# Performance work log

Hardware: AMD Instinct MI355X
Metric: run time of the kernel (lower is better)

Reference implementation:

```python
import jax, jax.numpy as jnp
import numpy as np

NUM_AGES = 100
FEAT_DIM = 512
BATCH = 4096
TEMPERATURE = 0.1
EPS = 1e-6


def setup_inputs() -> dict:
    key = jax.random.key(0)
    k1, k2, k3 = jax.random.split(key, 3)
    z_age = jax.random.normal(k1, (BATCH, FEAT_DIM), dtype=jnp.float32)
    ages = jax.random.randint(k2, (BATCH,), 0, NUM_AGES, dtype=jnp.int64)
    proxies = jax.random.normal(k3, (NUM_AGES, FEAT_DIM), dtype=jnp.float32)
    return {"z_age": z_age, "ages": ages, "proxies": proxies}


def _unit_diff(a, b):
    d = a - b
    return d / (jnp.linalg.norm(d, axis=-1, keepdims=True) + EPS)


def reference(z_age, ages, proxies):
    # Vectorized equivalent of the O(B^2) python double loop.
    # Only pairs with age_i < age_j contribute (age_i > age_j branch is a no-op `...`).
    B = z_age.shape[0]
    A = proxies.shape[0]
    aj = ages.astype(jnp.int32)
    c_cur = proxies[aj]                                   # [B, D]
    c_next = proxies[jnp.minimum(aj + 1, A - 1)]          # [B, D]
    c_prev = proxies[jnp.maximum(aj - 1, 0)]              # [B, D]
    vf = _unit_diff(c_next, c_cur)                        # forward direction per sample j
    vb = _unit_diff(c_prev, c_cur)                        # backward direction per sample j

    # Pairwise norms via Gram matrix: ||z_i - z_j||.
    G = z_age @ z_age.T                                   # [B, B]
    sq = jnp.diagonal(G)                                  # [B]
    d2 = jnp.maximum(sq[:, None] + sq[None, :] - 2.0 * G, 0.0)
    norm = jnp.sqrt(d2)                                   # [B, B]
    denom = norm + EPS

    # dot(v_d_ij, v_f_j) = (z_i . vf_j - z_j . vf_j) / (||z_i - z_j|| + eps)
    Gf = z_age @ vf.T                                     # [B, B], Gf[i, j] = z_i . vf_j
    Gb = z_age @ vb.T
    dot_f = (Gf - jnp.diagonal(Gf)[None, :]) / denom
    dot_b = (Gb - jnp.diagonal(Gb)[None, :]) / denom

    # -log(exp(df/T) / (exp(df/T) + exp(db/T))) = softplus((db - df)/T)
    per_pair = jax.nn.softplus((dot_b - dot_f) / TEMPERATURE)  # [B, B]
    mask = ages[:, None] < ages[None, :]
    loss = jnp.sum(jnp.where(mask, per_pair, 0.0))
    return loss / (B * (B - 1))
```

## Files before the change

kernel.cpp:

```cpp
#include <hip/hip_runtime.h>
#include <hip/hip_bf16.h>

#define NUM_AGES 100
#define FEAT 512
#define BATCH 4096
#define EPSF 1e-6f
#define INV_T 10.0f
#define INV_NORM (1.0f / ((float)BATCH * (float)(BATCH - 1)))

#define BM 128
#define BN 64
#define BK 32
#define NTILES 1056

typedef __bf16 bf16_t;
typedef __bf16 v8bf __attribute__((ext_vector_type(8)));
typedef float v4f __attribute__((ext_vector_type(4)));

__device__ __forceinline__ void async16(const void* g, void* l) {
  __builtin_amdgcn_global_load_lds(
      (const __attribute__((address_space(1))) void*)g,
      (__attribute__((address_space(3))) void*)l, 16, 0, 0);
}

__global__ __launch_bounds__(1024) void sort_kernel(
    const int* __restrict__ ages, int* __restrict__ perm, float* __restrict__ out)
{
  __shared__ int hist[NUM_AGES];
  __shared__ int base[NUM_AGES];
  int t = threadIdx.x;
  if (t == 0) out[0] = 0.0f;
  if (t < NUM_AGES) hist[t] = 0;
  __syncthreads();
  for (int j = t; j < BATCH; j += 1024) {
    int a = ages[j];
    a = a < 0 ? 0 : (a > NUM_AGES - 1 ? NUM_AGES - 1 : a);
    atomicAdd(&hist[a], 1);
  }
  __syncthreads();
  if (t == 0) {
    int s = 0;
    for (int a = 0; a < NUM_AGES; ++a) { base[a] = s; s += hist[a]; }
  }
  __syncthreads();
  for (int j = t; j < BATCH; j += 1024) {
    int a = ages[j];
    a = a < 0 ? 0 : (a > NUM_AGES - 1 ? NUM_AGES - 1 : a);
    int pos = atomicAdd(&base[a], 1);
    perm[pos] = j;
  }
}

__global__ __launch_bounds__(256) void prep_kernel(
    const float* __restrict__ z, const int* __restrict__ ages,
    const float* __restrict__ proxies, const int* __restrict__ perm,
    bf16_t* __restrict__ zb, bf16_t* __restrict__ wb,
    float* __restrict__ sq, float* __restrict__ hd,
    int* __restrict__ ages_s)
{
  int j = blockIdx.x;
  int s = perm[j];
  int t = threadIdx.x;
  int araw = ages[s];
  int a = araw < 0 ? 0 : (araw > NUM_AGES - 1 ? NUM_AGES - 1 : araw);
  const float* cc = proxies + (size_t)a * FEAT;
  const float* cn = proxies + (size_t)(a + 1 > NUM_AGES - 1 ? NUM_AGES - 1 : a + 1) * FEAT;
  const float* cp = proxies + (size_t)(a - 1 < 0 ? 0 : a - 1) * FEAT;
  const float* zr = z + (size_t)s * FEAT;

  float zf[2], dff[2], dbf[2];
  float s_ff = 0.f, s_bb = 0.f, s_zz = 0.f, s_zf = 0.f, s_zb = 0.f;
#pragma unroll
  for (int e = 0; e < 2; ++e) {
    int c = t + e * 256;
    float ccv = cc[c];
    dff[e] = cn[c] - ccv;
    dbf[e] = cp[c] - ccv;
    zf[e] = zr[c];
    s_ff += dff[e] * dff[e];
    s_bb += dbf[e] * dbf[e];
    s_zz += zf[e] * zf[e];
    s_zf += zf[e] * dff[e];
    s_zb += zf[e] * dbf[e];
  }
#pragma unroll
  for (int off = 32; off > 0; off >>= 1) {
    s_ff += __shfl_down(s_ff, off, 64);
    s_bb += __shfl_down(s_bb, off, 64);
    s_zz += __shfl_down(s_zz, off, 64);
    s_zf += __shfl_down(s_zf, off, 64);
    s_zb += __shfl_down(s_zb, off, 64);
  }
  __shared__ float red[4][5];
  int wv = t >> 6, lane = t & 63;
  if (lane == 0) {
    red[wv][0] = s_ff; red[wv][1] = s_bb; red[wv][2] = s_zz;
    red[wv][3] = s_zf; red[wv][4] = s_zb;
  }
  __syncthreads();
  float ff = red[0][0] + red[1][0] + red[2][0] + red[3][0];
  float bb = red[0][1] + red[1][1] + red[2][1] + red[3][1];
  float zz = red[0][2] + red[1][2] + red[2][2] + red[3][2];
  float zdf = red[0][3] + red[1][3] + red[2][3] + red[3][3];
  float zdb = red[0][4] + red[1][4] + red[2][4] + red[3][4];

  float rf = 1.0f / (sqrtf(ff) + EPSF);
  float rb = 1.0f / (sqrtf(bb) + EPSF);
  int key = (j >> 1) & 3;
#pragma unroll
  for (int e = 0; e < 2; ++e) {
    int c = t + e * 256;
    int c2 = (c & ~31) | (((((c >> 3) & 3) ^ key) << 3)) | (c & 7);
    float wval = dbf[e] * rb - dff[e] * rf;
    wb[(size_t)j * FEAT + c2] = (bf16_t)wval;
    zb[(size_t)j * FEAT + c2] = (bf16_t)zf[e];
  }
  if (t == 0) {
    sq[j] = zz;
    hd[j] = rb * zdb - rf * zdf;
    ages_s[j] = araw;
  }
}

__global__ __launch_bounds__(256, 4) void pair_kernel(
    const bf16_t* __restrict__ zb, const bf16_t* __restrict__ wb,
    const float* __restrict__ sq, const float* __restrict__ hd,
    const int* __restrict__ ages, float* __restrict__ out)
{
  __shared__ __attribute__((aligned(16))) char lds[16384];
  __shared__ float s_sqi[BM];
  __shared__ int   s_agei[BM];
  __shared__ float s_sqj[BN];
  __shared__ float s_hdj[BN];
  __shared__ int   s_agej[BN];
  __shared__ float wsum[4];

  int t = threadIdx.x;
  int wv = t >> 6, lane = t & 63;

  int rem = blockIdx.x;
  int by = 0;
  while (rem >= 64 - 2 * by) { rem -= 64 - 2 * by; ++by; }
  int bx = 2 * by + rem;
  int i0 = by * BM, j0 = bx * BN;

  if (t < BM) {
    s_sqi[t] = sq[i0 + t];
    s_agei[t] = ages[i0 + t];
  } else if (t < BM + BN) {
    int u = t - BM;
    s_sqj[u] = sq[j0 + u];
    s_hdj[u] = hd[j0 + u];
    s_agej[u] = ages[j0 + u];
  }

  v4f accG[4][2], accH[4][2];
#pragma unroll
  for (int a = 0; a < 4; ++a)
#pragma unroll
    for (int b = 0; b < 2; ++b) {
      accG[a][b] = (v4f){0.f, 0.f, 0.f, 0.f};
      accH[a][b] = (v4f){0.f, 0.f, 0.f, 0.f};
    }

  int wm = wv >> 1, wn = wv & 1;
  int lm = lane & 15, q = lane >> 4;
  int psw = (q ^ ((lm >> 1) & 3)) * 16;

  int grow = lane >> 2;
  int gcol = (lane & 3) * 8;

  const bf16_t* pA0 = zb + (size_t)(i0 + wv * 16 + grow) * FEAT + gcol;
  const bf16_t* pA1 = zb + (size_t)(i0 + 64 + wv * 16 + grow) * FEAT + gcol;
  const bf16_t* pZ  = zb + (size_t)(j0 + wv * 16 + grow) * FEAT + gcol;
  const bf16_t* pW  = wb + (size_t)(j0 + wv * 16 + grow) * FEAT + gcol;
  char* dA0 = lds + wv * 1024;
  char* dA1 = lds + 4096 + wv * 1024;
  char* dZ  = lds + 8192 + wv * 1024;
  char* dW  = lds + 12288 + wv * 1024;

  for (int k0 = 0; k0 < FEAT; k0 += BK) {
    async16(pA0, dA0);
    async16(pA1, dA1);
    async16(pZ, dZ);
    async16(pW, dW);
    pA0 += BK; pA1 += BK; pZ += BK; pW += BK;
    __syncthreads();

    v8bf afr[4], bz[2], bw[2];
#pragma unroll
    for (int mi = 0; mi < 4; ++mi) {
      int r = wm * 64 + mi * 16 + lm;
      afr[mi] = *(const v8bf*)(lds + r * 64 + psw);
    }
#pragma unroll
    for (int ni = 0; ni < 2; ++ni) {
      int r = wn * 32 + ni * 16 + lm;
      bz[ni] = *(const v8bf*)(lds + 8192 + r * 64 + psw);
      bw[ni] = *(const v8bf*)(lds + 12288 + r * 64 + psw);
    }
#pragma unroll
    for (int mi = 0; mi < 4; ++mi)
#pragma unroll
      for (int ni = 0; ni < 2; ++ni) {
        accG[mi][ni] = __builtin_amdgcn_mfma_f32_16x16x32_bf16(afr[mi], bz[ni], accG[mi][ni], 0, 0, 0);
        accH[mi][ni] = __builtin_amdgcn_mfma_f32_16x16x32_bf16(afr[mi], bw[ni], accH[mi][ni], 0, 0, 0);
      }
    __syncthreads();
  }

  float tsum = 0.f;
#pragma unroll
  for (int ni = 0; ni < 2; ++ni) {
    int jl = wn * 32 + ni * 16 + lm;
    float sqj = s_sqj[jl];
    float hdj = s_hdj[jl];
    int aj = s_agej[jl];
#pragma unroll
    for (int mi = 0; mi < 4; ++mi) {
#pragma unroll
      for (int r = 0; r < 4; ++r) {
        int il = wm * 64 + mi * 16 + q * 4 + r;
        float g = accG[mi][ni][r];
        float h = accH[mi][ni][r];
        float d2 = fmaxf(s_sqi[il] + sqj - 2.0f * g, 1e-12f);
        float rs = __builtin_amdgcn_rsqf(d2);
        float arg = (h - hdj) * INV_T * rs;
        float sp = fmaxf(arg, 0.0f) + __logf(1.0f + __expf(-fabsf(arg)));
        tsum += (s_agei[il] < aj) ? sp : 0.0f;
      }
    }
  }

#pragma unroll
  for (int off = 32; off > 0; off >>= 1) tsum += __shfl_down(tsum, off, 64);
  if (lane == 0) wsum[wv] = tsum;
  __syncthreads();
  if (t == 0)
    atomicAdd(out, (wsum[0] + wsum[1] + wsum[2] + wsum[3]) * INV_NORM);
}

extern "C" void kernel_launch(void* const* d_in, const int* in_sizes, int n_in,
                              void* d_out, int out_size, void* d_ws, size_t ws_size,
                              hipStream_t stream) {
  const float* z = (const float*)d_in[0];
  const int* ages = (const int*)d_in[1];
  const float* proxies = (const float*)d_in[2];
  float* out = (float*)d_out;

  char* ws = (char*)d_ws;
  bf16_t* zb = (bf16_t*)ws;
  bf16_t* wb = (bf16_t*)(ws + (size_t)4 * 1024 * 1024);
  size_t o = (size_t)8 * 1024 * 1024;
  float* sq      = (float*)(ws + o);
  float* hd      = (float*)(ws + o + 16384);
  int*   perm    = (int*)  (ws + o + 32768);
  int*   ages_s  = (int*)  (ws + o + 49152);

  sort_kernel<<<1, 1024, 0, stream>>>(ages, perm, out);
  prep_kernel<<<BATCH, 256, 0, stream>>>(z, ages, proxies, perm, zb, wb, sq, hd, ages_s);
  pair_kernel<<<NTILES, 256, 0, stream>>>(zb, wb, sq, hd, ages_s, out);
}
```

Measured before the change: 111.2 us.

## Fuse age sort into prep kernel via per-row rank counting

Removes the single-block histogram sort kernel and instead has each prep block compute its sample's sorted position by counting all samples with a smaller age (ties broken by index), then scatter its outputs to that rank. Output zeroing moves into the prep kernel too. This drops a serial single-block launch and the perm indirection, at the cost of every block scanning all 4096 ages (redundant O(B^2) integer work, mostly cached reads).

```diff
diff --git a/kernel.cpp b/kernel.cpp
--- a/kernel.cpp
+++ b/kernel.cpp
@@ -23,50 +23,31 @@
       (__attribute__((address_space(3))) void*)l, 16, 0, 0);
 }
 
-__global__ __launch_bounds__(1024) void sort_kernel(
-    const int* __restrict__ ages, int* __restrict__ perm, float* __restrict__ out)
-{
-  __shared__ int hist[NUM_AGES];
-  __shared__ int base[NUM_AGES];
-  int t = threadIdx.x;
-  if (t == 0) out[0] = 0.0f;
-  if (t < NUM_AGES) hist[t] = 0;
-  __syncthreads();
-  for (int j = t; j < BATCH; j += 1024) {
-    int a = ages[j];
-    a = a < 0 ? 0 : (a > NUM_AGES - 1 ? NUM_AGES - 1 : a);
-    atomicAdd(&hist[a], 1);
-  }
-  __syncthreads();
-  if (t == 0) {
-    int s = 0;
-    for (int a = 0; a < NUM_AGES; ++a) { base[a] = s; s += hist[a]; }
-  }
-  __syncthreads();
-  for (int j = t; j < BATCH; j += 1024) {
-    int a = ages[j];
-    a = a < 0 ? 0 : (a > NUM_AGES - 1 ? NUM_AGES - 1 : a);
-    int pos = atomicAdd(&base[a], 1);
-    perm[pos] = j;
-  }
-}
-
 __global__ __launch_bounds__(256) void prep_kernel(
     const float* __restrict__ z, const int* __restrict__ ages,
-    const float* __restrict__ proxies, const int* __restrict__ perm,
+    const float* __restrict__ proxies,
     bf16_t* __restrict__ zb, bf16_t* __restrict__ wb,
     float* __restrict__ sq, float* __restrict__ hd,
-    int* __restrict__ ages_s)
+    int* __restrict__ ages_s, float* __restrict__ out)
 {
   int j = blockIdx.x;
-  int s = perm[j];
   int t = threadIdx.x;
-  int araw = ages[s];
+  if (j == 0 && t == 0) out[0] = 0.0f;
+
+  int araw = ages[j];
   int a = araw < 0 ? 0 : (araw > NUM_AGES - 1 ? NUM_AGES - 1 : araw);
   const float* cc = proxies + (size_t)a * FEAT;
   const float* cn = proxies + (size_t)(a + 1 > NUM_AGES - 1 ? NUM_AGES - 1 : a + 1) * FEAT;
   const float* cp = proxies + (size_t)(a - 1 < 0 ? 0 : a - 1) * FEAT;
-  const float* zr = z + (size_t)s * FEAT;
+  const float* zr = z + (size_t)j * FEAT;
+
+  int cnt = 0;
+#pragma unroll
+  for (int e = 0; e < BATCH / 256; ++e) {
+    int k = t + e * 256;
+    int ak = ages[k];
+    cnt += (ak < araw || (ak == araw && k < j)) ? 1 : 0;
+  }
 
   float zf[2], dff[2], dbf[2];
   float s_ff = 0.f, s_bb = 0.f, s_zz = 0.f, s_zf = 0.f, s_zb = 0.f;
@@ -83,6 +64,7 @@
     s_zf += zf[e] * dff[e];
     s_zb += zf[e] * dbf[e];
   }
+  float fcnt = (float)cnt;
 #pragma unroll
   for (int off = 32; off > 0; off >>= 1) {
     s_ff += __shfl_down(s_ff, off, 64);
@@ -90,12 +72,13 @@
     s_zz += __shfl_down(s_zz, off, 64);
     s_zf += __shfl_down(s_zf, off, 64);
     s_zb += __shfl_down(s_zb, off, 64);
-  }
-  __shared__ float red[4][5];
+    fcnt += __shfl_down(fcnt, off, 64);
+  }
+  __shared__ float red[4][6];
   int wv = t >> 6, lane = t & 63;
   if (lane == 0) {
     red[wv][0] = s_ff; red[wv][1] = s_bb; red[wv][2] = s_zz;
-    red[wv][3] = s_zf; red[wv][4] = s_zb;
+    red[wv][3] = s_zf; red[wv][4] = s_zb; red[wv][5] = fcnt;
   }
   __syncthreads();
   float ff = red[0][0] + red[1][0] + red[2][0] + red[3][0];
@@ -103,22 +86,23 @@
   float zz = red[0][2] + red[1][2] + red[2][2] + red[3][2];
   float zdf = red[0][3] + red[1][3] + red[2][3] + red[3][3];
   float zdb = red[0][4] + red[1][4] + red[2][4] + red[3][4];
+  int rank = (int)(red[0][5] + red[1][5] + red[2][5] + red[3][5]);
 
   float rf = 1.0f / (sqrtf(ff) + EPSF);
   float rb = 1.0f / (sqrtf(bb) + EPSF);
-  int key = (j >> 1) & 3;
+  int key = (rank >> 1) & 3;
 #pragma unroll
   for (int e = 0; e < 2; ++e) {
     int c = t + e * 256;
     int c2 = (c & ~31) | (((((c >> 3) & 3) ^ key) << 3)) | (c & 7);
     float wval = dbf[e] * rb - dff[e] * rf;
-    wb[(size_t)j * FEAT + c2] = (bf16_t)wval;
-    zb[(size_t)j * FEAT + c2] = (bf16_t)zf[e];
+    wb[(size_t)rank * FEAT + c2] = (bf16_t)wval;
+    zb[(size_t)rank * FEAT + c2] = (bf16_t)zf[e];
   }
   if (t == 0) {
-    sq[j] = zz;
-    hd[j] = rb * zdb - rf * zdf;
-    ages_s[j] = araw;
+    sq[rank] = zz;
+    hd[rank] = rb * zdb - rf * zdf;
+    ages_s[rank] = araw;
   }
 }
 
@@ -254,10 +238,8 @@
   size_t o = (size_t)8 * 1024 * 1024;
   float* sq      = (float*)(ws + o);
   float* hd      = (float*)(ws + o + 16384);
-  int*   perm    = (int*)  (ws + o + 32768);
-  int*   ages_s  = (int*)  (ws + o + 49152);
-
-  sort_kernel<<<1, 1024, 0, stream>>>(ages, perm, out);
-  prep_kernel<<<BATCH, 256, 0, stream>>>(z, ages, proxies, perm, zb, wb, sq, hd, ages_s);
+  int*   ages_s  = (int*)  (ws + o + 32768);
+
+  prep_kernel<<<BATCH, 256, 0, stream>>>(z, ages, proxies, zb, wb, sq, hd, ages_s, out);
   pair_kernel<<<NTILES, 256, 0, stream>>>(zb, wb, sq, hd, ages_s, out);
 }
```

Result: faster. 106.3 us (-4.4%).
